# Kernel optimization log

Measured on AMD Instinct MI355X. Metric: run time of the kernel, lower is better.

Reference implementation:

```python
import jax, jax.numpy as jnp
import numpy as np

N, E, F, R = 10000, 320000, 128, 20


def _cross_dim1(a, b):
    # a: [E,3,F], b: [E,3,1]; cross product along axis 1 (broadcast over F)
    return jnp.stack([
        a[:, 1] * b[:, 2] - a[:, 2] * b[:, 1],
        a[:, 2] * b[:, 0] - a[:, 0] * b[:, 2],
        a[:, 0] * b[:, 1] - a[:, 1] * b[:, 0],
    ], axis=1)


def setup_inputs() -> dict:
    key = jax.random.key(0)
    ks = jax.random.split(key, 15)
    s = jax.random.normal(ks[0], (N, F), jnp.float32)
    v = jax.random.normal(ks[1], (N, 3, F), jnp.float32)
    re1 = jax.random.normal(ks[2], (E, R), jnp.float32)
    re2 = jax.random.normal(ks[3], (E, R), jnp.float32)
    f1 = jax.random.uniform(ks[4], (E,), jnp.float32)
    f2 = jax.random.uniform(ks[5], (E,), jnp.float32)
    u1 = jax.random.normal(ks[6], (E, 3), jnp.float32)
    u2 = jax.random.normal(ks[7], (E, 3), jnp.float32)
    edge_index = jax.random.randint(ks[8], (2, E), 0, N, jnp.int32)
    # mlp_phi: Linear(F,F) -> SiLU -> Linear(F,6F); linear_W: Linear(R,6F)
    W1 = jax.random.normal(ks[9], (F, F), jnp.float32) / np.sqrt(F)
    b1 = jnp.zeros((F,), jnp.float32)
    W2 = jax.random.normal(ks[10], (F, 6 * F), jnp.float32) / np.sqrt(F)
    b2 = jnp.zeros((6 * F,), jnp.float32)
    Wr = jax.random.normal(ks[11], (R, 6 * F), jnp.float32) / np.sqrt(R)
    br = jnp.zeros((6 * F,), jnp.float32)
    return dict(s=s, v=v, radial_embeddings_1=re1, radial_embeddings_2=re2,
                f_cut_1=f1, f_cut_2=f2, unit_vectors_1=u1, unit_vectors_2=u2,
                edge_index=edge_index, W1=W1, b1=b1, W2=W2, b2=b2, Wr=Wr, br=br)


def reference(s, v, radial_embeddings_1, radial_embeddings_2, f_cut_1, f_cut_2,
              unit_vectors_1, unit_vectors_2, edge_index, W1, b1, W2, b2, Wr, br):
    idx_i, idx_j = edge_index[0], edge_index[1]
    n_nodes = s.shape[0]
    nf = W1.shape[0]
    # phi: [N, 6F]
    phi = jax.nn.silu(s @ W1 + b1) @ W2 + b2
    # radial gate: [E, 6F]
    W = (radial_embeddings_1 @ Wr + br) * f_cut_1[:, None] \
        + (radial_embeddings_2 @ Wr + br) * f_cut_2[:, None]
    x = phi[idx_j] * W  # [E, 6F]
    x_s, x_vv, x_vs_1, x_vs_2, x_vc_1, x_vc_2 = [
        x[:, i * nf:(i + 1) * nf] for i in range(6)
    ]
    ds = jax.ops.segment_sum(x_s, idx_i, num_segments=n_nodes)  # [N,F]
    v_j = v[idx_j]  # [E,3,F]
    u1 = unit_vectors_1[:, :, None]  # [E,3,1]
    u2 = unit_vectors_2[:, :, None]
    x_v = (v_j * x_vv[:, None, :]
           + x_vs_1[:, None, :] * u1
           + x_vs_2[:, None, :] * u2
           + x_vc_1[:, None, :] * _cross_dim1(v_j, u1)
           + x_vc_2[:, None, :] * _cross_dim1(v_j, u2))  # [E,3,F]
    dv = jax.ops.segment_sum(x_v, idx_i, num_segments=n_nodes)  # [N,3,F]
    return (s + ds, v + dv)
```

## Files before the change

### kernel.cpp

```cpp
#include <hip/hip_runtime.h>
#include <hip/hip_bf16.h>

#define NN   10000
#define NE   320000
#define NF   128
#define SIXF 768
#define K21  21

typedef unsigned short u16;
typedef unsigned int   u32;

__device__ __forceinline__ float bf2f_lo(u32 pk) { return __uint_as_float(pk << 16); }
__device__ __forceinline__ float bf2f_hi(u32 pk) { return __uint_as_float(pk & 0xffff0000u); }
__device__ __forceinline__ u16 f2bf(float f) {
    u32 x = __float_as_uint(f);
    return (u16)((x + 0x7fffu + ((x >> 16) & 1u)) >> 16);
}

__global__ __launch_bounds__(256) void init_out_kernel(
    const float4* __restrict__ s4, const float4* __restrict__ v4, float4* __restrict__ out4)
{
    int i = blockIdx.x * 256 + threadIdx.x;
    if (i < NN * NF / 4) out4[i] = s4[i];
    else                 out4[i] = v4[i - NN * NF / 4];
}

__global__ __launch_bounds__(256) void phi_kernel(
    const float* __restrict__ s, const float* __restrict__ W1, const float* __restrict__ b1,
    const float* __restrict__ W2, const float* __restrict__ b2, u16* __restrict__ phiw)
{
    __shared__ float sh[32][NF];
    __shared__ float hh[32][NF];
    const int t = threadIdx.x;
    const int row0 = blockIdx.x * 32;

    for (int i = t; i < 32 * NF / 4; i += 256) {
        int r = i >> 5, c4 = i & 31;
        float4 val = make_float4(0.f, 0.f, 0.f, 0.f);
        if (row0 + r < NN) val = *reinterpret_cast<const float4*>(&s[(size_t)(row0 + r) * NF + c4 * 4]);
        *reinterpret_cast<float4*>(&sh[r][c4 * 4]) = val;
    }
    __syncthreads();
    {
        const int c = t & 127;
        const int half = t >> 7;
        float hacc[16];
        #pragma unroll
        for (int i = 0; i < 16; ++i) hacc[i] = 0.f;
        for (int k4 = 0; k4 < 32; ++k4) {
            float w0 = W1[(k4 * 4 + 0) * NF + c];
            float w1 = W1[(k4 * 4 + 1) * NF + c];
            float w2 = W1[(k4 * 4 + 2) * NF + c];
            float w3 = W1[(k4 * 4 + 3) * NF + c];
            #pragma unroll
            for (int rr = 0; rr < 16; ++rr) {
                float4 sv = *reinterpret_cast<const float4*>(&sh[half * 16 + rr][k4 * 4]);
                hacc[rr] = fmaf(sv.x, w0, hacc[rr]);
                hacc[rr] = fmaf(sv.y, w1, hacc[rr]);
                hacc[rr] = fmaf(sv.z, w2, hacc[rr]);
                hacc[rr] = fmaf(sv.w, w3, hacc[rr]);
            }
        }
        float b1c = b1[c];
        #pragma unroll
        for (int rr = 0; rr < 16; ++rr) {
            float x = hacc[rr] + b1c;
            float sg = 1.0f / (1.0f + __expf(-x));
            hh[half * 16 + rr][c] = x * sg;
        }
    }
    __syncthreads();
    {
        float pa[32][3];
        #pragma unroll
        for (int r = 0; r < 32; ++r)
            #pragma unroll
            for (int cg = 0; cg < 3; ++cg) pa[r][cg] = 0.f;

        for (int k4 = 0; k4 < 32; ++k4) {
            float w[4][3];
            #pragma unroll
            for (int kk = 0; kk < 4; ++kk)
                #pragma unroll
                for (int cg = 0; cg < 3; ++cg)
                    w[kk][cg] = W2[(size_t)(k4 * 4 + kk) * SIXF + t + 256 * cg];
            #pragma unroll
            for (int r = 0; r < 32; ++r) {
                float4 hv = *reinterpret_cast<const float4*>(&hh[r][k4 * 4]);
                #pragma unroll
                for (int cg = 0; cg < 3; ++cg) {
                    pa[r][cg] = fmaf(hv.x, w[0][cg], pa[r][cg]);
                    pa[r][cg] = fmaf(hv.y, w[1][cg], pa[r][cg]);
                    pa[r][cg] = fmaf(hv.z, w[2][cg], pa[r][cg]);
                    pa[r][cg] = fmaf(hv.w, w[3][cg], pa[r][cg]);
                }
            }
        }
        float b2c[3] = { b2[t], b2[t + 256], b2[t + 512] };
        #pragma unroll
        for (int r = 0; r < 32; ++r) {
            if (row0 + r < NN) {
                #pragma unroll
                for (int cg = 0; cg < 3; ++cg)
                    phiw[(size_t)(row0 + r) * SIXF + t + 256 * cg] = f2bf(pa[r][cg] + b2c[cg]);
            }
        }
    }
}

__global__ __launch_bounds__(256) void prep_wrb_kernel(
    const float* __restrict__ Wr, const float* __restrict__ br, u16* __restrict__ wrb)
{
    int i = blockIdx.x * 256 + threadIdx.x;
    if (i < 21 * SIXF) wrb[i] = f2bf(i < 20 * SIXF ? Wr[i] : br[i - 20 * SIXF]);
}

__global__ __launch_bounds__(256) void prep_vbf_kernel(
    const float* __restrict__ v, u16* __restrict__ vbf)
{
    int i = blockIdx.x * 256 + threadIdx.x;
    if (i < NN * 384) vbf[i] = f2bf(v[i]);
}

__global__ __launch_bounds__(256) void zero_cnt_kernel(int* __restrict__ cnt) {
    int i = blockIdx.x * 256 + threadIdx.x;
    if (i < NN) cnt[i] = 0;
}

__global__ __launch_bounds__(256) void hist_kernel(const int* __restrict__ eidx, int* __restrict__ cnt) {
    int e = blockIdx.x * 256 + threadIdx.x;
    if (e < NE) atomicAdd(&cnt[eidx[e]], 1);
}

__global__ __launch_bounds__(256) void scan_kernel(const int* __restrict__ cnt, int* __restrict__ offs) {
    __shared__ int part[256];
    const int t = threadIdx.x;
    int lsum = 0;
    if (t < 250) {
        #pragma unroll 4
        for (int k = 0; k < 40; ++k) lsum += cnt[t * 40 + k];
    }
    part[t] = lsum;
    __syncthreads();
    if (t == 0) {
        int run = 0;
        for (int i = 0; i < 250; ++i) { int c = part[i]; part[i] = run; run += c; }
    }
    __syncthreads();
    if (t < 250) {
        int run = part[t];
        for (int k = 0; k < 40; ++k) {
            int idx = t * 40 + k;
            offs[idx] = run;
            run += cnt[idx];
        }
    }
}

__global__ __launch_bounds__(256) void scatter_kernel(
    const int* __restrict__ eidx, int* __restrict__ offs, int* __restrict__ elist) {
    int e = blockIdx.x * 256 + threadIdx.x;
    if (e < NE) {
        int pos = atomicAdd(&offs[eidx[e]], 1);
        elist[pos] = e;
    }
}

template<bool USE_VBF>
__global__ __launch_bounds__(256, 4) void gather_kernel(
    const float* __restrict__ re1, const float* __restrict__ re2,
    const float* __restrict__ f1, const float* __restrict__ f2,
    const float* __restrict__ u1v, const float* __restrict__ u2v,
    const int* __restrict__ eidx,
    const u16* __restrict__ phiw, const float* __restrict__ v,
    const u16* __restrict__ vbf, const u16* __restrict__ wrb,
    const float* __restrict__ s,
    const int* __restrict__ cnt, const int* __restrict__ offs,
    const int* __restrict__ elist,
    float* __restrict__ out)
{
    __shared__ u16   WrB[K21][SIXF];
    __shared__ float smem[2048];
    float (*rrs)[K21] = (float(*)[K21])smem;
    float (*euv)[6]   = (float(*)[6])(smem + 672);
    int*   ejd        = (int*)(smem + 864);
    float (*redbuf)[512] = (float(*)[512])smem;

    const int t = threadIdx.x;
    const int node = blockIdx.x;
    const int deg   = cnt[node];
    const int end   = offs[node];
    const int start = end - deg;

    {
        const u32* wg = (const u32*)wrb;
        u32* wl = (u32*)&WrB[0][0];
        for (int i = t; i < 8064; i += 256) wl[i] = wg[i];
    }

    const int wave = t >> 6, lane = t & 63;
    float accS[2] = {0.f, 0.f};
    float accV[3][2] = {{0.f,0.f},{0.f,0.f},{0.f,0.f}};

    for (int base = 0; base < deg; base += 32) {
        const int m = min(32, deg - base);
        __syncthreads();
        for (int i = t; i < m * K21; i += 256) {
            int el = i / K21, r = i - el * K21;
            int e = elist[start + base + el];
            float a;
            if (r < 20) a = f1[e] * re1[(size_t)e * 20 + r] + f2[e] * re2[(size_t)e * 20 + r];
            else        a = f1[e] + f2[e];
            rrs[el][r] = a;
        }
        if (t < m) {
            int e = elist[start + base + t];
            ejd[t] = eidx[NE + e];
            #pragma unroll
            for (int d = 0; d < 3; ++d) {
                euv[t][d]     = u1v[(size_t)e * 3 + d];
                euv[t][3 + d] = u2v[(size_t)e * 3 + d];
            }
        }
        __syncthreads();

        #pragma unroll 1
        for (int half = 0; half < 2; ++half) {
            const int eg = wave * 8 + half * 4;
            if (eg >= m) continue;
            float acc[4][12];
            #pragma unroll
            for (int ea = 0; ea < 4; ++ea)
                #pragma unroll
                for (int cb = 0; cb < 12; ++cb) acc[ea][cb] = 0.f;

            for (int r = 0; r < K21; ++r) {
                float wv[12];
                #pragma unroll
                for (int cc = 0; cc < 6; ++cc) {
                    u32 pk = *reinterpret_cast<const u32*>(&WrB[r][cc * 128 + 2 * lane]);
                    wv[2 * cc]     = bf2f_lo(pk);
                    wv[2 * cc + 1] = bf2f_hi(pk);
                }
                #pragma unroll
                for (int e4 = 0; e4 < 4; ++e4) {
                    float a = rrs[eg + e4][r];
                    #pragma unroll
                    for (int c = 0; c < 12; ++c) acc[e4][c] = fmaf(a, wv[c], acc[e4][c]);
                }
            }

            #pragma unroll
            for (int e4 = 0; e4 < 4; ++e4) {
                const int el = eg + e4;
                if (el < m) {
                    const int nj = ejd[el];
                    const float u1x = euv[el][0], u1y = euv[el][1], u1z = euv[el][2];
                    const float u2x = euv[el][3], u2y = euv[el][4], u2z = euv[el][5];
                    const u16* ph = phiw + (size_t)nj * SIXF + 2 * lane;
                    float px[12];
                    #pragma unroll
                    for (int cc = 0; cc < 6; ++cc) {
                        u32 pk = *reinterpret_cast<const u32*>(ph + cc * 128);
                        px[2 * cc]     = bf2f_lo(pk);
                        px[2 * cc + 1] = bf2f_hi(pk);
                    }
                    float2 va, vb, vc;
                    if (USE_VBF) {
                        const u16* vj = vbf + (size_t)nj * 384 + 2 * lane;
                        u32 p0 = *reinterpret_cast<const u32*>(vj);
                        u32 p1 = *reinterpret_cast<const u32*>(vj + 128);
                        u32 p2 = *reinterpret_cast<const u32*>(vj + 256);
                        va = make_float2(bf2f_lo(p0), bf2f_hi(p0));
                        vb = make_float2(bf2f_lo(p1), bf2f_hi(p1));
                        vc = make_float2(bf2f_lo(p2), bf2f_hi(p2));
                    } else {
                        const float* vj = v + (size_t)nj * 384 + 2 * lane;
                        va = *reinterpret_cast<const float2*>(vj);
                        vb = *reinterpret_cast<const float2*>(vj + 128);
                        vc = *reinterpret_cast<const float2*>(vj + 256);
                    }
                    #pragma unroll
                    for (int ff = 0; ff < 2; ++ff) {
                        float xs   = acc[e4][0 + ff]  * px[0 + ff];
                        float xvv  = acc[e4][2 + ff]  * px[2 + ff];
                        float xvs1 = acc[e4][4 + ff]  * px[4 + ff];
                        float xvs2 = acc[e4][6 + ff]  * px[6 + ff];
                        float xvc1 = acc[e4][8 + ff]  * px[8 + ff];
                        float xvc2 = acc[e4][10 + ff] * px[10 + ff];
                        float a0 = ff ? va.y : va.x;
                        float a1 = ff ? vb.y : vb.x;
                        float a2 = ff ? vc.y : vc.x;
                        float c1x = a1 * u1z - a2 * u1y;
                        float c1y = a2 * u1x - a0 * u1z;
                        float c1z = a0 * u1y - a1 * u1x;
                        float c2x = a1 * u2z - a2 * u2y;
                        float c2y = a2 * u2x - a0 * u2z;
                        float c2z = a0 * u2y - a1 * u2x;
                        accS[ff] += xs;
                        accV[0][ff] += a0 * xvv + xvs1 * u1x + xvs2 * u2x + xvc1 * c1x + xvc2 * c2x;
                        accV[1][ff] += a1 * xvv + xvs1 * u1y + xvs2 * u2y + xvc1 * c1y + xvc2 * c2y;
                        accV[2][ff] += a2 * xvv + xvs1 * u1z + xvs2 * u2z + xvc1 * c1z + xvc2 * c2z;
                    }
                }
            }
        }
    }

    __syncthreads();
    #pragma unroll
    for (int ff = 0; ff < 2; ++ff) {
        redbuf[wave][2 * lane + ff] = accS[ff];
        #pragma unroll
        for (int d = 0; d < 3; ++d)
            redbuf[wave][128 + d * 128 + 2 * lane + ff] = accV[d][ff];
    }
    __syncthreads();
    for (int k = t; k < 512; k += 256) {
        float sum = redbuf[0][k] + redbuf[1][k] + redbuf[2][k] + redbuf[3][k];
        if (k < NF) {
            out[(size_t)node * NF + k] = s[(size_t)node * NF + k] + sum;
        } else {
            int kv = k - NF;
            out[(size_t)NN * NF + (size_t)node * 384 + kv] = v[(size_t)node * 384 + kv] + sum;
        }
    }
}

__global__ __launch_bounds__(256) void edge_kernel(
    const float* __restrict__ re1, const float* __restrict__ re2,
    const float* __restrict__ f1, const float* __restrict__ f2,
    const float* __restrict__ u1v, const float* __restrict__ u2v,
    const int* __restrict__ eidx,
    const u16* __restrict__ phiw, const float* __restrict__ v,
    const float* __restrict__ Wr, const float* __restrict__ br,
    float* __restrict__ out)
{
    __shared__ u16   WrB[K21][SIXF];
    __shared__ float rrs[32][K21];
    __shared__ float euv[32][6];
    __shared__ int   eid[32][2];
    const int t = threadIdx.x;
    const int e0 = blockIdx.x * 32;

    for (int i = t; i < 20 * SIXF; i += 256) WrB[0][i] = f2bf(Wr[i]);
    for (int c = t; c < SIXF; c += 256)      WrB[20][c] = f2bf(br[c]);
    for (int i = t; i < 32 * K21; i += 256) {
        int el = i / K21, r = i - el * K21;
        int e = e0 + el;
        float a;
        if (r < 20) a = f1[e] * re1[(size_t)e * 20 + r] + f2[e] * re2[(size_t)e * 20 + r];
        else        a = f1[e] + f2[e];
        rrs[el][r] = a;
    }
    if (t < 32) {
        int e = e0 + t;
        eid[t][0] = eidx[e];
        eid[t][1] = eidx[NE + e];
        #pragma unroll
        for (int d = 0; d < 3; ++d) {
            euv[t][d]     = u1v[(size_t)e * 3 + d];
            euv[t][3 + d] = u2v[(size_t)e * 3 + d];
        }
    }
    __syncthreads();

    const int wave = t >> 6, lane = t & 63;
    #pragma unroll 1
    for (int half = 0; half < 2; ++half) {
        const int eg = wave * 8 + half * 4;
        float acc[4][12];
        #pragma unroll
        for (int ea = 0; ea < 4; ++ea)
            #pragma unroll
            for (int cb = 0; cb < 12; ++cb) acc[ea][cb] = 0.f;

        for (int r = 0; r < K21; ++r) {
            float wv[12];
            #pragma unroll
            for (int cc = 0; cc < 6; ++cc) {
                u32 pk = *reinterpret_cast<const u32*>(&WrB[r][cc * 128 + 2 * lane]);
                wv[2 * cc]     = bf2f_lo(pk);
                wv[2 * cc + 1] = bf2f_hi(pk);
            }
            #pragma unroll
            for (int e4 = 0; e4 < 4; ++e4) {
                float a = rrs[eg + e4][r];
                #pragma unroll
                for (int c = 0; c < 12; ++c) acc[e4][c] = fmaf(a, wv[c], acc[e4][c]);
            }
        }

        #pragma unroll
        for (int e4 = 0; e4 < 4; ++e4) {
            const int el = eg + e4;
            const int ni = eid[el][0], nj = eid[el][1];
            const float u1x = euv[el][0], u1y = euv[el][1], u1z = euv[el][2];
            const float u2x = euv[el][3], u2y = euv[el][4], u2z = euv[el][5];
            const u16* ph = phiw + (size_t)nj * SIXF + 2 * lane;
            float px[12];
            #pragma unroll
            for (int cc = 0; cc < 6; ++cc) {
                u32 pk = *reinterpret_cast<const u32*>(ph + cc * 128);
                px[2 * cc]     = bf2f_lo(pk);
                px[2 * cc + 1] = bf2f_hi(pk);
            }
            const float* vj = v + (size_t)nj * 384 + 2 * lane;
            float2 va = *reinterpret_cast<const float2*>(vj);
            float2 vb = *reinterpret_cast<const float2*>(vj + 128);
            float2 vc = *reinterpret_cast<const float2*>(vj + 256);
            float* po = out + (size_t)ni * NF + 2 * lane;
            float* pv = out + (size_t)NN * NF + (size_t)ni * 384 + 2 * lane;
            #pragma unroll
            for (int ff = 0; ff < 2; ++ff) {
                float xs   = acc[e4][0 + ff]  * px[0 + ff];
                float xvv  = acc[e4][2 + ff]  * px[2 + ff];
                float xvs1 = acc[e4][4 + ff]  * px[4 + ff];
                float xvs2 = acc[e4][6 + ff]  * px[6 + ff];
                float xvc1 = acc[e4][8 + ff]  * px[8 + ff];
                float xvc2 = acc[e4][10 + ff] * px[10 + ff];
                float a0 = ff ? va.y : va.x;
                float a1 = ff ? vb.y : vb.x;
                float a2 = ff ? vc.y : vc.x;
                float c1x = a1 * u1z - a2 * u1y;
                float c1y = a2 * u1x - a0 * u1z;
                float c1z = a0 * u1y - a1 * u1x;
                float c2x = a1 * u2z - a2 * u2y;
                float c2y = a2 * u2x - a0 * u2z;
                float c2z = a0 * u2y - a1 * u2x;
                float xv0 = a0 * xvv + xvs1 * u1x + xvs2 * u2x + xvc1 * c1x + xvc2 * c2x;
                float xv1 = a1 * xvv + xvs1 * u1y + xvs2 * u2y + xvc1 * c1y + xvc2 * c2y;
                float xv2 = a2 * xvv + xvs1 * u1z + xvs2 * u2z + xvc1 * c1z + xvc2 * c2z;
                unsafeAtomicAdd(po + ff, xs);
                unsafeAtomicAdd(pv + ff, xv0);
                unsafeAtomicAdd(pv + 128 + ff, xv1);
                unsafeAtomicAdd(pv + 256 + ff, xv2);
            }
        }
    }
}

extern "C" void kernel_launch(void* const* d_in, const int* in_sizes, int n_in,
                              void* d_out, int out_size, void* d_ws, size_t ws_size,
                              hipStream_t stream) {
    const float* s   = (const float*)d_in[0];
    const float* v   = (const float*)d_in[1];
    const float* re1 = (const float*)d_in[2];
    const float* re2 = (const float*)d_in[3];
    const float* f1  = (const float*)d_in[4];
    const float* f2  = (const float*)d_in[5];
    const float* u1  = (const float*)d_in[6];
    const float* u2  = (const float*)d_in[7];
    const int*   ei  = (const int*)d_in[8];
    const float* W1  = (const float*)d_in[9];
    const float* b1  = (const float*)d_in[10];
    const float* W2  = (const float*)d_in[11];
    const float* b2  = (const float*)d_in[12];
    const float* Wr  = (const float*)d_in[13];
    const float* br  = (const float*)d_in[14];
    float* out = (float*)d_out;

    const size_t PHI_B  = (size_t)NN * SIXF * 2;
    const size_t VBF_B  = (size_t)NN * 384 * 2;
    const size_t CNT_B  = (size_t)NN * 4;
    const size_t EL_B   = (size_t)NE * 4;
    const size_t WRB_B  = (size_t)21 * SIXF * 2;

    const size_t need_full = PHI_B + VBF_B + 2 * CNT_B + EL_B + WRB_B;
    const size_t need_csr  = PHI_B + 2 * CNT_B + EL_B + WRB_B;

    u16* phiw = (u16*)d_ws;
    phi_kernel<<<dim3((NN + 31) / 32), dim3(256), 0, stream>>>(s, W1, b1, W2, b2, phiw);

    if (ws_size >= need_full) {
        u16* vbf   = (u16*)((char*)d_ws + PHI_B);
        int* cnt   = (int*)((char*)d_ws + PHI_B + VBF_B);
        int* offs  = cnt + NN;
        int* elist = offs + NN;
        u16* wrb   = (u16*)((char*)elist + EL_B);

        prep_wrb_kernel<<<dim3((21 * SIXF + 255) / 256), dim3(256), 0, stream>>>(Wr, br, wrb);
        prep_vbf_kernel<<<dim3((NN * 384 + 255) / 256), dim3(256), 0, stream>>>(v, vbf);
        zero_cnt_kernel<<<dim3((NN + 255) / 256), dim3(256), 0, stream>>>(cnt);
        hist_kernel<<<dim3((NE + 255) / 256), dim3(256), 0, stream>>>(ei, cnt);
        scan_kernel<<<dim3(1), dim3(256), 0, stream>>>(cnt, offs);
        scatter_kernel<<<dim3((NE + 255) / 256), dim3(256), 0, stream>>>(ei, offs, elist);
        gather_kernel<true><<<dim3(NN), dim3(256), 0, stream>>>(
            re1, re2, f1, f2, u1, u2, ei, phiw, v, vbf, wrb, s, cnt, offs, elist, out);
    } else if (ws_size >= need_csr) {
        int* cnt   = (int*)((char*)d_ws + PHI_B);
        int* offs  = cnt + NN;
        int* elist = offs + NN;
        u16* wrb   = (u16*)((char*)elist + EL_B);

        prep_wrb_kernel<<<dim3((21 * SIXF + 255) / 256), dim3(256), 0, stream>>>(Wr, br, wrb);
        zero_cnt_kernel<<<dim3((NN + 255) / 256), dim3(256), 0, stream>>>(cnt);
        hist_kernel<<<dim3((NE + 255) / 256), dim3(256), 0, stream>>>(ei, cnt);
        scan_kernel<<<dim3(1), dim3(256), 0, stream>>>(cnt, offs);
        scatter_kernel<<<dim3((NE + 255) / 256), dim3(256), 0, stream>>>(ei, offs, elist);
        gather_kernel<false><<<dim3(NN), dim3(256), 0, stream>>>(
            re1, re2, f1, f2, u1, u2, ei, phiw, v, (const u16*)nullptr, wrb, s, cnt, offs, elist, out);
    } else {
        init_out_kernel<<<dim3((NN * NF + NN * 3 * NF) / 4 / 256), dim3(256), 0, stream>>>(
            (const float4*)s, (const float4*)v, (float4*)out);
        edge_kernel<<<dim3(NE / 32), dim3(256), 0, stream>>>(
            re1, re2, f1, f2, u1, u2, ei, phiw, v, Wr, br, out);
    }
}
```

Baseline: 539.7 us.

## Use fp16 dot2 for radial gate, precompute packed radial inputs, shrink LDS and phi tiles

The radial-gate matmul in the gather kernel now uses packed fp16 pairs and v_dot2 instructions, replacing bf16-to-fp32 unpacking and scalar FMAs. The weights are stored as 11 row-pairs, and a new pre-pass packs the scaled radial embeddings per edge into fp16 pairs. LDS use drops, which may allow more blocks per CU. Several smaller changes ride along: the phi kernel tile goes from 32 to 16 rows, the count array is cleared with a memset, the four-wave reduction becomes a two-stage one, and the fp32-v fallback path is removed. fp16 has a narrower exponent range than bf16, so very large or very small radial values risk accuracy issues. The extra pre-pass adds a separate write and read of about 14 MB.

```diff
diff --git a/kernel.cpp b/kernel.cpp
--- a/kernel.cpp
+++ b/kernel.cpp
@@ -6,9 +6,11 @@
 #define NF   128
 #define SIXF 768
 #define K21  21
+#define NRP  11
 
 typedef unsigned short u16;
 typedef unsigned int   u32;
+typedef _Float16 h2 __attribute__((ext_vector_type(2)));
 
 __device__ __forceinline__ float bf2f_lo(u32 pk) { return __uint_as_float(pk << 16); }
 __device__ __forceinline__ float bf2f_hi(u32 pk) { return __uint_as_float(pk & 0xffff0000u); }
@@ -16,6 +18,10 @@
     u32 x = __float_as_uint(f);
     return (u16)((x + 0x7fffu + ((x >> 16) & 1u)) >> 16);
 }
+__device__ __forceinline__ u32 pkh2(float a, float b) {
+    h2 h = { (_Float16)a, (_Float16)b };
+    return __builtin_bit_cast(u32, h);
+}
 
 __global__ __launch_bounds__(256) void init_out_kernel(
     const float4* __restrict__ s4, const float4* __restrict__ v4, float4* __restrict__ out4)
@@ -29,12 +35,12 @@
     const float* __restrict__ s, const float* __restrict__ W1, const float* __restrict__ b1,
     const float* __restrict__ W2, const float* __restrict__ b2, u16* __restrict__ phiw)
 {
-    __shared__ float sh[32][NF];
-    __shared__ float hh[32][NF];
+    __shared__ float sh[16][NF];
+    __shared__ float hh[16][NF];
     const int t = threadIdx.x;
-    const int row0 = blockIdx.x * 32;
-
-    for (int i = t; i < 32 * NF / 4; i += 256) {
+    const int row0 = blockIdx.x * 16;
+
+    for (int i = t; i < 16 * NF / 4; i += 256) {
         int r = i >> 5, c4 = i & 31;
         float4 val = make_float4(0.f, 0.f, 0.f, 0.f);
         if (row0 + r < NN) val = *reinterpret_cast<const float4*>(&s[(size_t)(row0 + r) * NF + c4 * 4]);
@@ -44,17 +50,17 @@
     {
         const int c = t & 127;
         const int half = t >> 7;
-        float hacc[16];
-        #pragma unroll
-        for (int i = 0; i < 16; ++i) hacc[i] = 0.f;
+        float hacc[8];
+        #pragma unroll
+        for (int i = 0; i < 8; ++i) hacc[i] = 0.f;
         for (int k4 = 0; k4 < 32; ++k4) {
             float w0 = W1[(k4 * 4 + 0) * NF + c];
             float w1 = W1[(k4 * 4 + 1) * NF + c];
             float w2 = W1[(k4 * 4 + 2) * NF + c];
             float w3 = W1[(k4 * 4 + 3) * NF + c];
             #pragma unroll
-            for (int rr = 0; rr < 16; ++rr) {
-                float4 sv = *reinterpret_cast<const float4*>(&sh[half * 16 + rr][k4 * 4]);
+            for (int rr = 0; rr < 8; ++rr) {
+                float4 sv = *reinterpret_cast<const float4*>(&sh[half * 8 + rr][k4 * 4]);
                 hacc[rr] = fmaf(sv.x, w0, hacc[rr]);
                 hacc[rr] = fmaf(sv.y, w1, hacc[rr]);
                 hacc[rr] = fmaf(sv.z, w2, hacc[rr]);
@@ -63,17 +69,17 @@
         }
         float b1c = b1[c];
         #pragma unroll
-        for (int rr = 0; rr < 16; ++rr) {
+        for (int rr = 0; rr < 8; ++rr) {
             float x = hacc[rr] + b1c;
             float sg = 1.0f / (1.0f + __expf(-x));
-            hh[half * 16 + rr][c] = x * sg;
+            hh[half * 8 + rr][c] = x * sg;
         }
     }
     __syncthreads();
     {
-        float pa[32][3];
-        #pragma unroll
-        for (int r = 0; r < 32; ++r)
+        float pa[16][3];
+        #pragma unroll
+        for (int r = 0; r < 16; ++r)
             #pragma unroll
             for (int cg = 0; cg < 3; ++cg) pa[r][cg] = 0.f;
 
@@ -85,7 +91,7 @@
                 for (int cg = 0; cg < 3; ++cg)
                     w[kk][cg] = W2[(size_t)(k4 * 4 + kk) * SIXF + t + 256 * cg];
             #pragma unroll
-            for (int r = 0; r < 32; ++r) {
+            for (int r = 0; r < 16; ++r) {
                 float4 hv = *reinterpret_cast<const float4*>(&hh[r][k4 * 4]);
                 #pragma unroll
                 for (int cg = 0; cg < 3; ++cg) {
@@ -98,7 +104,7 @@
         }
         float b2c[3] = { b2[t], b2[t + 256], b2[t + 512] };
         #pragma unroll
-        for (int r = 0; r < 32; ++r) {
+        for (int r = 0; r < 16; ++r) {
             if (row0 + r < NN) {
                 #pragma unroll
                 for (int cg = 0; cg < 3; ++cg)
@@ -108,11 +114,38 @@
     }
 }
 
-__global__ __launch_bounds__(256) void prep_wrb_kernel(
-    const float* __restrict__ Wr, const float* __restrict__ br, u16* __restrict__ wrb)
+__global__ __launch_bounds__(256) void prep_wrbp_kernel(
+    const float* __restrict__ Wr, const float* __restrict__ br, u32* __restrict__ wrbp)
 {
     int i = blockIdx.x * 256 + threadIdx.x;
-    if (i < 21 * SIXF) wrb[i] = f2bf(i < 20 * SIXF ? Wr[i] : br[i - 20 * SIXF]);
+    if (i < NRP * SIXF) {
+        int rp = i / SIXF, col = i - rp * SIXF;
+        float v0 = (rp < 10) ? Wr[(size_t)(2 * rp) * SIXF + col] : br[col];
+        float v1 = (rp < 10) ? Wr[(size_t)(2 * rp + 1) * SIXF + col] : 0.f;
+        wrbp[i] = pkh2(v0, v1);
+    }
+}
+
+__global__ __launch_bounds__(256) void prep_rre_kernel(
+    const float* __restrict__ re1, const float* __restrict__ re2,
+    const float* __restrict__ f1, const float* __restrict__ f2,
+    u32* __restrict__ rre)
+{
+    int i = blockIdx.x * 256 + threadIdx.x;
+    if (i < NE * NRP) {
+        int e = i / NRP, rp = i - e * NRP;
+        float a0, a1;
+        float c1 = f1[e], c2 = f2[e];
+        if (rp < 10) {
+            int r = 2 * rp;
+            a0 = c1 * re1[(size_t)e * 20 + r]     + c2 * re2[(size_t)e * 20 + r];
+            a1 = c1 * re1[(size_t)e * 20 + r + 1] + c2 * re2[(size_t)e * 20 + r + 1];
+        } else {
+            a0 = c1 + c2;
+            a1 = 0.f;
+        }
+        rre[i] = pkh2(a0, a1);
+    }
 }
 
 __global__ __launch_bounds__(256) void prep_vbf_kernel(
@@ -120,11 +153,6 @@
 {
     int i = blockIdx.x * 256 + threadIdx.x;
     if (i < NN * 384) vbf[i] = f2bf(v[i]);
-}
-
-__global__ __launch_bounds__(256) void zero_cnt_kernel(int* __restrict__ cnt) {
-    int i = blockIdx.x * 256 + threadIdx.x;
-    if (i < NN) cnt[i] = 0;
 }
 
 __global__ __launch_bounds__(256) void hist_kernel(const int* __restrict__ eidx, int* __restrict__ cnt) {
@@ -166,24 +194,25 @@
     }
 }
 
-template<bool USE_VBF>
+template<bool RRE>
 __global__ __launch_bounds__(256, 4) void gather_kernel(
     const float* __restrict__ re1, const float* __restrict__ re2,
     const float* __restrict__ f1, const float* __restrict__ f2,
     const float* __restrict__ u1v, const float* __restrict__ u2v,
     const int* __restrict__ eidx,
     const u16* __restrict__ phiw, const float* __restrict__ v,
-    const u16* __restrict__ vbf, const u16* __restrict__ wrb,
+    const u16* __restrict__ vbf, const u32* __restrict__ wrbp,
+    const u32* __restrict__ rre,
     const float* __restrict__ s,
     const int* __restrict__ cnt, const int* __restrict__ offs,
     const int* __restrict__ elist,
     float* __restrict__ out)
 {
-    __shared__ u16   WrB[K21][SIXF];
-    __shared__ float smem[2048];
-    float (*rrs)[K21] = (float(*)[K21])smem;
-    float (*euv)[6]   = (float(*)[6])(smem + 672);
-    int*   ejd        = (int*)(smem + 864);
+    __shared__ u32   WrBp[NRP][SIXF];
+    __shared__ float smem[1024];
+    u32*   rrsp = (u32*)smem;
+    float (*euv)[6] = (float(*)[6])(smem + 352);
+    int*   ejd      = (int*)(smem + 544);
     float (*redbuf)[512] = (float(*)[512])smem;
 
     const int t = threadIdx.x;
@@ -192,11 +221,7 @@
     const int end   = offs[node];
     const int start = end - deg;
 
-    {
-        const u32* wg = (const u32*)wrb;
-        u32* wl = (u32*)&WrB[0][0];
-        for (int i = t; i < 8064; i += 256) wl[i] = wg[i];
-    }
+    for (int i = t; i < NRP * SIXF; i += 256) WrBp[0][i] = wrbp[i];
 
     const int wave = t >> 6, lane = t & 63;
     float accS[2] = {0.f, 0.f};
@@ -205,13 +230,21 @@
     for (int base = 0; base < deg; base += 32) {
         const int m = min(32, deg - base);
         __syncthreads();
-        for (int i = t; i < m * K21; i += 256) {
-            int el = i / K21, r = i - el * K21;
+        for (int i = t; i < m * NRP; i += 256) {
+            int el = i / NRP, rp = i - el * NRP;
             int e = elist[start + base + el];
-            float a;
-            if (r < 20) a = f1[e] * re1[(size_t)e * 20 + r] + f2[e] * re2[(size_t)e * 20 + r];
-            else        a = f1[e] + f2[e];
-            rrs[el][r] = a;
+            if (RRE) {
+                rrsp[el * NRP + rp] = rre[(size_t)e * NRP + rp];
+            } else {
+                float a0, a1;
+                float c1 = f1[e], c2 = f2[e];
+                if (rp < 10) {
+                    int r = 2 * rp;
+                    a0 = c1 * re1[(size_t)e * 20 + r]     + c2 * re2[(size_t)e * 20 + r];
+                    a1 = c1 * re1[(size_t)e * 20 + r + 1] + c2 * re2[(size_t)e * 20 + r + 1];
+                } else { a0 = c1 + c2; a1 = 0.f; }
+                rrsp[el * NRP + rp] = pkh2(a0, a1);
+            }
         }
         if (t < m) {
             int e = elist[start + base + t];
@@ -234,19 +267,21 @@
                 #pragma unroll
                 for (int cb = 0; cb < 12; ++cb) acc[ea][cb] = 0.f;
 
-            for (int r = 0; r < K21; ++r) {
-                float wv[12];
+            for (int rp = 0; rp < NRP; ++rp) {
+                h2 a[4];
+                #pragma unroll
+                for (int e4 = 0; e4 < 4; ++e4)
+                    a[e4] = __builtin_bit_cast(h2, rrsp[(eg + e4) * NRP + rp]);
                 #pragma unroll
                 for (int cc = 0; cc < 6; ++cc) {
-                    u32 pk = *reinterpret_cast<const u32*>(&WrB[r][cc * 128 + 2 * lane]);
-                    wv[2 * cc]     = bf2f_lo(pk);
-                    wv[2 * cc + 1] = bf2f_hi(pk);
-                }
-                #pragma unroll
-                for (int e4 = 0; e4 < 4; ++e4) {
-                    float a = rrs[eg + e4][r];
+                    uint2 p = *reinterpret_cast<const uint2*>(&WrBp[rp][cc * 128 + 2 * lane]);
+                    h2 w0 = __builtin_bit_cast(h2, p.x);
+                    h2 w1 = __builtin_bit_cast(h2, p.y);
                     #pragma unroll
-                    for (int c = 0; c < 12; ++c) acc[e4][c] = fmaf(a, wv[c], acc[e4][c]);
+                    for (int e4 = 0; e4 < 4; ++e4) {
+                        acc[e4][2 * cc]     = __builtin_amdgcn_fdot2(a[e4], w0, acc[e4][2 * cc],     false);
+                        acc[e4][2 * cc + 1] = __builtin_amdgcn_fdot2(a[e4], w1, acc[e4][2 * cc + 1], false);
+                    }
                 }
             }
 
@@ -265,21 +300,13 @@
                         px[2 * cc]     = bf2f_lo(pk);
                         px[2 * cc + 1] = bf2f_hi(pk);
                     }
-                    float2 va, vb, vc;
-                    if (USE_VBF) {
-                        const u16* vj = vbf + (size_t)nj * 384 + 2 * lane;
-                        u32 p0 = *reinterpret_cast<const u32*>(vj);
-                        u32 p1 = *reinterpret_cast<const u32*>(vj + 128);
-                        u32 p2 = *reinterpret_cast<const u32*>(vj + 256);
-                        va = make_float2(bf2f_lo(p0), bf2f_hi(p0));
-                        vb = make_float2(bf2f_lo(p1), bf2f_hi(p1));
-                        vc = make_float2(bf2f_lo(p2), bf2f_hi(p2));
-                    } else {
-                        const float* vj = v + (size_t)nj * 384 + 2 * lane;
-                        va = *reinterpret_cast<const float2*>(vj);
-                        vb = *reinterpret_cast<const float2*>(vj + 128);
-                        vc = *reinterpret_cast<const float2*>(vj + 256);
-                    }
+                    const u16* vj = vbf + (size_t)nj * 384 + 2 * lane;
+                    u32 p0 = *reinterpret_cast<const u32*>(vj);
+                    u32 p1 = *reinterpret_cast<const u32*>(vj + 128);
+                    u32 p2 = *reinterpret_cast<const u32*>(vj + 256);
+                    float2 va = make_float2(bf2f_lo(p0), bf2f_hi(p0));
+                    float2 vb = make_float2(bf2f_lo(p1), bf2f_hi(p1));
+                    float2 vc = make_float2(bf2f_lo(p2), bf2f_hi(p2));
                     #pragma unroll
                     for (int ff = 0; ff < 2; ++ff) {
                         float xs   = acc[e4][0 + ff]  * px[0 + ff];
@@ -308,16 +335,28 @@
     }
 
     __syncthreads();
-    #pragma unroll
-    for (int ff = 0; ff < 2; ++ff) {
-        redbuf[wave][2 * lane + ff] = accS[ff];
-        #pragma unroll
-        for (int d = 0; d < 3; ++d)
-            redbuf[wave][128 + d * 128 + 2 * lane + ff] = accV[d][ff];
+    if (wave >= 2) {
+        #pragma unroll
+        for (int ff = 0; ff < 2; ++ff) {
+            redbuf[wave - 2][2 * lane + ff] = accS[ff];
+            #pragma unroll
+            for (int d = 0; d < 3; ++d)
+                redbuf[wave - 2][128 + d * 128 + 2 * lane + ff] = accV[d][ff];
+        }
+    }
+    __syncthreads();
+    if (wave < 2) {
+        #pragma unroll
+        for (int ff = 0; ff < 2; ++ff) {
+            redbuf[wave][2 * lane + ff] += accS[ff];
+            #pragma unroll
+            for (int d = 0; d < 3; ++d)
+                redbuf[wave][128 + d * 128 + 2 * lane + ff] += accV[d][ff];
+        }
     }
     __syncthreads();
     for (int k = t; k < 512; k += 256) {
-        float sum = redbuf[0][k] + redbuf[1][k] + redbuf[2][k] + redbuf[3][k];
+        float sum = redbuf[0][k] + redbuf[1][k];
         if (k < NF) {
             out[(size_t)node * NF + k] = s[(size_t)node * NF + k] + sum;
         } else {
@@ -464,42 +503,38 @@
     const size_t VBF_B  = (size_t)NN * 384 * 2;
     const size_t CNT_B  = (size_t)NN * 4;
     const size_t EL_B   = (size_t)NE * 4;
-    const size_t WRB_B  = (size_t)21 * SIXF * 2;
-
-    const size_t need_full = PHI_B + VBF_B + 2 * CNT_B + EL_B + WRB_B;
-    const size_t need_csr  = PHI_B + 2 * CNT_B + EL_B + WRB_B;
+    const size_t WRBP_B = (size_t)NRP * SIXF * 4;
+    const size_t RRE_B  = (size_t)NE * NRP * 4;
+
+    const size_t need_t2 = PHI_B + VBF_B + 2 * CNT_B + EL_B + WRBP_B;
+    const size_t need_t1 = need_t2 + RRE_B;
 
     u16* phiw = (u16*)d_ws;
-    phi_kernel<<<dim3((NN + 31) / 32), dim3(256), 0, stream>>>(s, W1, b1, W2, b2, phiw);
-
-    if (ws_size >= need_full) {
+    phi_kernel<<<dim3((NN + 15) / 16), dim3(256), 0, stream>>>(s, W1, b1, W2, b2, phiw);
+
+    if (ws_size >= need_t2) {
         u16* vbf   = (u16*)((char*)d_ws + PHI_B);
         int* cnt   = (int*)((char*)d_ws + PHI_B + VBF_B);
         int* offs  = cnt + NN;
         int* elist = offs + NN;
-        u16* wrb   = (u16*)((char*)elist + EL_B);
-
-        prep_wrb_kernel<<<dim3((21 * SIXF + 255) / 256), dim3(256), 0, stream>>>(Wr, br, wrb);
+        u32* wrbp  = (u32*)((char*)elist + EL_B);
+        u32* rre   = (u32*)((char*)wrbp + WRBP_B);
+
+        prep_wrbp_kernel<<<dim3((NRP * SIXF + 255) / 256), dim3(256), 0, stream>>>(Wr, br, wrbp);
         prep_vbf_kernel<<<dim3((NN * 384 + 255) / 256), dim3(256), 0, stream>>>(v, vbf);
-        zero_cnt_kernel<<<dim3((NN + 255) / 256), dim3(256), 0, stream>>>(cnt);
+        hipMemsetAsync(cnt, 0, CNT_B, stream);
         hist_kernel<<<dim3((NE + 255) / 256), dim3(256), 0, stream>>>(ei, cnt);
         scan_kernel<<<dim3(1), dim3(256), 0, stream>>>(cnt, offs);
         scatter_kernel<<<dim3((NE + 255) / 256), dim3(256), 0, stream>>>(ei, offs, elist);
-        gather_kernel<true><<<dim3(NN), dim3(256), 0, stream>>>(
-            re1, re2, f1, f2, u1, u2, ei, phiw, v, vbf, wrb, s, cnt, offs, elist, out);
-    } else if (ws_size >= need_csr) {
-        int* cnt   = (int*)((char*)d_ws + PHI_B);
-        int* offs  = cnt + NN;
-        int* elist = offs + NN;
-        u16* wrb   = (u16*)((char*)elist + EL_B);
-
-        prep_wrb_kernel<<<dim3((21 * SIXF + 255) / 256), dim3(256), 0, stream>>>(Wr, br, wrb);
-        zero_cnt_kernel<<<dim3((NN + 255) / 256), dim3(256), 0, stream>>>(cnt);
-        hist_kernel<<<dim3((NE + 255) / 256), dim3(256), 0, stream>>>(ei, cnt);
-        scan_kernel<<<dim3(1), dim3(256), 0, stream>>>(cnt, offs);
-        scatter_kernel<<<dim3((NE + 255) / 256), dim3(256), 0, stream>>>(ei, offs, elist);
-        gather_kernel<false><<<dim3(NN), dim3(256), 0, stream>>>(
-            re1, re2, f1, f2, u1, u2, ei, phiw, v, (const u16*)nullptr, wrb, s, cnt, offs, elist, out);
+
+        if (ws_size >= need_t1) {
+            prep_rre_kernel<<<dim3((NE * NRP + 255) / 256), dim3(256), 0, stream>>>(re1, re2, f1, f2, rre);
+            gather_kernel<true><<<dim3(NN), dim3(256), 0, stream>>>(
+                re1, re2, f1, f2, u1, u2, ei, phiw, v, vbf, wrbp, rre, s, cnt, offs, elist, out);
+        } else {
+            gather_kernel<false><<<dim3(NN), dim3(256), 0, stream>>>(
+                re1, re2, f1, f2, u1, u2, ei, phiw, v, vbf, wrbp, (const u32*)nullptr, s, cnt, offs, elist, out);
+        }
     } else {
         init_out_kernel<<<dim3((NN * NF + NN * 3 * NF) / 4 / 256), dim3(256), 0, stream>>>(
             (const float4*)s, (const float4*)v, (float4*)out);
```

After: 1.901 ms. +252.2%, slower.
